# Optimization experiments

Measured on AMD Instinct MI355X. Metric: run time of the kernel, lower is better.

## Reference

```python
import jax, jax.numpy as jnp
import numpy as np

N = 20000      # total residues (nodes)
E = 320000     # contact edges
G = 16         # graphs in batch
D_IN = 1280    # ESM embedding dim
H = 256        # hidden channels (1=2=3)
C = 500        # GO classes
EPS = 1e-5


def setup_inputs() -> dict:
    key = jax.random.key(0)
    ks = jax.random.split(key, 16)
    s = 0.02
    return {
        "x": jax.random.normal(ks[0], (N, D_IN), jnp.float32),
        "edge_index": jax.random.randint(ks[1], (2, E), 0, N, jnp.int32),
        "edge_attr": jax.random.uniform(ks[2], (E, 1), jnp.float32),
        "batch": jnp.sort(jax.random.randint(ks[3], (N,), 0, G, jnp.int32)),
        "seq_emb": jax.random.normal(ks[4], (G, D_IN), jnp.float32),
        "W1": jax.random.normal(ks[5], (D_IN, H), jnp.float32) * s,
        "b1": jnp.zeros((H,), jnp.float32),
        "g1": jnp.ones((H,), jnp.float32),
        "be1": jnp.zeros((H,), jnp.float32),
        "W2": jax.random.normal(ks[6], (H, H), jnp.float32) * s,
        "b2": jnp.zeros((H,), jnp.float32),
        "g2": jnp.ones((H,), jnp.float32),
        "be2": jnp.zeros((H,), jnp.float32),
        "W3": jax.random.normal(ks[7], (H, H), jnp.float32) * s,
        "b3": jnp.zeros((H,), jnp.float32),
        "g3": jnp.ones((H,), jnp.float32),
        "be3": jnp.zeros((H,), jnp.float32),
        "fc1_w": jax.random.normal(ks[8], (D_IN, H), jnp.float32) * s,
        "fc1_b": jnp.zeros((H,), jnp.float32),
        "lin_w": jax.random.normal(ks[9], (H, C), jnp.float32) * s,
        "lin_b": jnp.zeros((C,), jnp.float32),
    }


def gcn_conv(x, row, col, ew, W, b):
    # PyG GCNConv: x' = D^{-1/2} (A + I) D^{-1/2} X W + b, with edge weights,
    # self-loops of weight 1, aggregation at target (col).
    xw = x @ W                                             # [N, H]
    deg = jax.ops.segment_sum(ew, col, num_segments=N) + 1.0
    dinv = jax.lax.rsqrt(deg)                              # [N]
    norm = dinv[row] * ew * dinv[col]                      # [E]
    agg = jax.ops.segment_sum(norm[:, None] * xw[row], col, num_segments=N)
    agg = agg + (dinv * dinv)[:, None] * xw                # self-loop term
    return agg + b


def batch_norm(x, g, b):
    # training-mode BN over the node dimension (biased variance, as torch)
    m = jnp.mean(x, axis=0)
    v = jnp.var(x, axis=0)
    return (x - m) * jax.lax.rsqrt(v + EPS) * g + b


def reference(x, edge_index, edge_attr, batch, seq_emb,
              W1, b1, g1, be1, W2, b2, g2, be2, W3, b3, g3, be3,
              fc1_w, fc1_b, lin_w, lin_b):
    row, col = edge_index[0], edge_index[1]
    ew = edge_attr[:, 0]

    h = batch_norm(jax.nn.relu(gcn_conv(x, row, col, ew, W1, b1)), g1, be1)
    h = batch_norm(jax.nn.relu(gcn_conv(h, row, col, ew, W2, b2)), g2, be2)
    h = batch_norm(gcn_conv(h, row, col, ew, W3, b3), g3, be3)

    # global_mean_pool over graphs
    sums = jax.ops.segment_sum(h, batch, num_segments=G)        # [G, H]
    cnt = jax.ops.segment_sum(jnp.ones((h.shape[0],), h.dtype), batch, num_segments=G)
    pooled = sums / jnp.maximum(cnt, 1.0)[:, None]

    y = seq_emb @ fc1_w + fc1_b                                 # [G, H]
    out = pooled + y
    # dropout skipped (eval mode)
    out = out @ lin_w + lin_b                                   # [G, C]
    return jax.nn.sigmoid(out)
```

## Files before the change

### kernel.cpp

```cpp
#include <hip/hip_runtime.h>
#include <hip/hip_bf16.h>
#include <math.h>

#define Nn 20000
#define En 320000
#define Gn 16
#define DINn 1280
#define Hn 256
#define Cn 500
#define EPSn 1e-5f
#define BNB 1024
#define SCB 256
#define SNB ((Nn + SCB - 1) / SCB)

typedef __attribute__((ext_vector_type(8))) short bf16x8;
typedef __attribute__((ext_vector_type(4))) float f32x4;

__device__ __forceinline__ float b2f(ushort u) {
    return __uint_as_float(((unsigned int)u) << 16);
}
__device__ __forceinline__ ushort f2b(float f) {
    __hip_bfloat16 h = __float2bfloat16(f);
    return *reinterpret_cast<ushort*>(&h);
}

#define GLOAD16(g, l) __builtin_amdgcn_global_load_lds( \
    (const __attribute__((address_space(1))) unsigned int*)(g), \
    (__attribute__((address_space(3))) unsigned int*)(l), 16, 0, 0)


__global__ void k_deg(const int* col, const float* ew, float* deg) {
    int e = blockIdx.x * blockDim.x + threadIdx.x;
    if (e < En) atomicAdd(&deg[col[e]], ew[e]);
}

__global__ void k_dinv(const float* deg, float* dinv, float* dinv2) {
    int i = blockIdx.x * blockDim.x + threadIdx.x;
    if (i < Nn) {
        float d = deg[i] + 1.0f;
        float r = rsqrtf(d);
        dinv[i] = r;
        dinv2[i] = 1.0f / d;
    }
}

__global__ void k_norm_count(const int* row, const int* col, const float* ew,
                             const float* dinv, float* normE, int* counts) {
    int e = blockIdx.x * blockDim.x + threadIdx.x;
    if (e < En) {
        int r = row[e], c = col[e];
        normE[e] = dinv[r] * ew[e] * dinv[c];
        atomicAdd(&counts[c], 1);
    }
}


__global__ __launch_bounds__(SCB) void k_scanA(const int* __restrict__ counts,
                                               int* __restrict__ excl,
                                               int* __restrict__ blocksum) {
    __shared__ int sd[SCB];
    int t = threadIdx.x, b = blockIdx.x;
    int i = b * SCB + t;
    int v = (i < Nn) ? counts[i] : 0;
    sd[t] = v;
    __syncthreads();
    #pragma unroll
    for (int o = 1; o < SCB; o <<= 1) {
        int tv = (t >= o) ? sd[t - o] : 0;
        __syncthreads();
        sd[t] += tv;
        __syncthreads();
    }
    if (i < Nn) excl[i] = sd[t] - v;
    if (t == SCB - 1) blocksum[b] = sd[t];
}

__global__ __launch_bounds__(128) void k_scanB(const int* __restrict__ blocksum,
                                               int* __restrict__ blockoff,
                                               int* __restrict__ offsets) {
    __shared__ int sd[128];
    int t = threadIdx.x;
    int v = (t < SNB) ? blocksum[t] : 0;
    sd[t] = v;
    __syncthreads();
    #pragma unroll
    for (int o = 1; o < 128; o <<= 1) {
        int tv = (t >= o) ? sd[t - o] : 0;
        __syncthreads();
        sd[t] += tv;
        __syncthreads();
    }
    if (t < SNB) blockoff[t] = sd[t] - v;
    if (t == SNB - 1) offsets[Nn] = sd[t];
}

__global__ __launch_bounds__(SCB) void k_scanC(const int* __restrict__ excl,
                                               const int* __restrict__ blockoff,
                                               int* __restrict__ offsets,
                                               int* __restrict__ cursor) {
    int b = blockIdx.x;
    int i = b * SCB + threadIdx.x;
    if (i < Nn) {
        int o = excl[i] + blockoff[b];
        offsets[i] = o;
        cursor[i] = o;
    }
}

__global__ void k_fill(const int* row, const int* col, const float* normE,
                       int* cursor, int* csr_row, float* csr_w) {
    int e = blockIdx.x * blockDim.x + threadIdx.x;
    if (e < En) {
        int c = col[e];
        int p = atomicAdd(&cursor[c], 1);
        csr_row[p] = row[e];
        csr_w[p] = normE[e];
    }
}


__global__ void k_gbounds(const int* __restrict__ batch, int* __restrict__ gstart) {
    int i = blockIdx.x * blockDim.x + threadIdx.x;
    if (i >= Nn) return;
    int b = batch[i];
    if (i == 0) {
        for (int g = 0; g <= b; g++) gstart[g] = 0;
    } else {
        int pb = batch[i - 1];
        for (int g = pb + 1; g <= b; g++) gstart[g] = i;
    }
    if (i == Nn - 1) {
        for (int g = b + 1; g <= Gn; g++) gstart[g] = Nn;
    }
}


__global__ __launch_bounds__(256) void k_x2bf(const float* __restrict__ x,
                                              ushort* __restrict__ xb) {
    size_t i = ((size_t)blockIdx.x * blockDim.x + threadIdx.x) * 8;
    const float4* xp = reinterpret_cast<const float4*>(&x[i]);
    float4 a = xp[0], b = xp[1];
    ushort t[8];
    t[0] = f2b(a.x); t[1] = f2b(a.y); t[2] = f2b(a.z); t[3] = f2b(a.w);
    t[4] = f2b(b.x); t[5] = f2b(b.y); t[6] = f2b(b.z); t[7] = f2b(b.w);
    *reinterpret_cast<uint4*>(&xb[i]) = *reinterpret_cast<uint4*>(&t[0]);
}


__global__ __launch_bounds__(256) void k_wt(const float* __restrict__ W,
                                            ushort* __restrict__ WT, int K) {
    __shared__ float tile[32][33];
    int k0 = blockIdx.x * 32, n0 = blockIdx.y * 32;
    int tx = threadIdx.x, ty = threadIdx.y;
    #pragma unroll
    for (int i = 0; i < 32; i += 8)
        tile[ty + i][tx] = W[(size_t)(k0 + ty + i) * Hn + n0 + tx];
    __syncthreads();
    #pragma unroll
    for (int i = 0; i < 32; i += 8)
        WT[(size_t)(n0 + ty + i) * K + k0 + tx] = f2b(tile[tx][ty + i]);
}


__global__ __launch_bounds__(256) void k_wtb(const float* __restrict__ W,
                                             const float* __restrict__ scaleA,
                                             const float* __restrict__ shiftA,
                                             ushort* __restrict__ WT,
                                             float* __restrict__ bv) {
    __shared__ float tile[32][33];
    int k0 = blockIdx.x * 32, n0 = blockIdx.y * 32;
    int tx = threadIdx.x, ty = threadIdx.y;
    #pragma unroll
    for (int i = 0; i < 32; i += 8)
        tile[ty + i][tx] = W[(size_t)(k0 + ty + i) * Hn + n0 + tx];
    __syncthreads();
    float sc = scaleA[k0 + tx], sh = shiftA[k0 + tx];
    #pragma unroll
    for (int i = 0; i < 32; i += 8) {
        float w = tile[tx][ty + i];
        WT[(size_t)(n0 + ty + i) * Hn + k0 + tx] = f2b(w * sc);
        float pb = w * sh;
        #pragma unroll
        for (int o = 16; o > 0; o >>= 1) pb += __shfl_down(pb, o, 32);
        if (tx == 0) atomicAdd(&bv[n0 + ty + i], pb);
    }
}


#define GBM 64
#define GBN 128
#define GBK 64

__global__ __launch_bounds__(256) void k_gemm_bf(
    const ushort* __restrict__ A, const ushort* __restrict__ BT,
    ushort* __restrict__ C, int M, int K)
{
    __shared__ ushort Asl[GBM][GBK];
    __shared__ ushort Bsl[GBN][GBK];
    const int bm = blockIdx.x * GBM;
    const int bn = blockIdx.y * GBN;
    const int tid = threadIdx.x;
    const int lane = tid & 63;
    const int wid = tid >> 6;
    const int wm = wid >> 1, wn = wid & 1;
    const int l15 = lane & 15, l16 = lane >> 4;

    const int lrow = lane >> 3;
    const int lcolb = 16 * ((lane & 7) ^ lrow);

    f32x4 acc[2][4] = {};
    const int nt = K / GBK;

    for (int t = 0; t < nt; t++) {
        const int k0 = t * GBK;
        #pragma unroll
        for (int c = 0; c < 2; c++) {
            int chunk = wid * 2 + c;
            int grow = bm + chunk * 8 + lrow;
            if (grow >= M) grow = M - 1;
            const char* src = (const char*)&A[(size_t)grow * K + k0] + lcolb;
            GLOAD16(src, &Asl[chunk * 8][0]);
        }
        #pragma unroll
        for (int c = 0; c < 4; c++) {
            int chunk = wid * 4 + c;
            int grow = bn + chunk * 8 + lrow;
            const char* src = (const char*)&BT[(size_t)grow * K + k0] + lcolb;
            GLOAD16(src, &Bsl[chunk * 8][0]);
        }
        __syncthreads();

        #pragma unroll
        for (int ks = 0; ks < 2; ks++) {
            bf16x8 afr[2], bfr[4];
            #pragma unroll
            for (int i = 0; i < 2; i++) {
                int r = wm * 32 + i * 16 + l15;
                int cb = (ks * 64 + l16 * 16) ^ ((r & 7) << 4);
                afr[i] = *reinterpret_cast<const bf16x8*>((const char*)&Asl[r][0] + cb);
            }
            #pragma unroll
            for (int j = 0; j < 4; j++) {
                int r = wn * 64 + j * 16 + l15;
                int cb = (ks * 64 + l16 * 16) ^ ((r & 7) << 4);
                bfr[j] = *reinterpret_cast<const bf16x8*>((const char*)&Bsl[r][0] + cb);
            }
            #pragma unroll
            for (int i = 0; i < 2; i++)
                #pragma unroll
                for (int j = 0; j < 4; j++)
                    acc[i][j] = __builtin_amdgcn_mfma_f32_16x16x32_bf16(afr[i], bfr[j], acc[i][j], 0, 0, 0);
        }
        __syncthreads();
    }

    #pragma unroll
    for (int i = 0; i < 2; i++) {
        #pragma unroll
        for (int r = 0; r < 4; r++) {
            int grow = bm + wm * 32 + i * 16 + l16 * 4 + r;
            if (grow < M) {
                #pragma unroll
                for (int j = 0; j < 4; j++)
                    C[(size_t)grow * Hn + bn + wn * 64 + j * 16 + l15] = f2b(acc[i][j][r]);
            }
        }
    }
}


__device__ __forceinline__ void agg_accum(float* acc, float w, const uint4& v) {
    unsigned int u;
    u = v.x; acc[0] += w * b2f((ushort)u); acc[1] += w * b2f((ushort)(u >> 16));
    u = v.y; acc[2] += w * b2f((ushort)u); acc[3] += w * b2f((ushort)(u >> 16));
    u = v.z; acc[4] += w * b2f((ushort)u); acc[5] += w * b2f((ushort)(u >> 16));
    u = v.w; acc[6] += w * b2f((ushort)u); acc[7] += w * b2f((ushort)(u >> 16));
}

__global__ __launch_bounds__(256) void k_agg(const ushort* __restrict__ xw,
                                             const int* __restrict__ offsets,
                                             const int* __restrict__ csr_row,
                                             const float* __restrict__ csr_w,
                                             const float* __restrict__ dinv2,
                                             const float* __restrict__ bias,
                                             const float* __restrict__ bv,
                                             ushort* __restrict__ outp, int do_relu) {
    int node = blockIdx.x * 8 + (threadIdx.x >> 5);
    int l32 = threadIdx.x & 31;
    int s = offsets[node], e = offsets[node + 1];
    const uint4* xw4 = reinterpret_cast<const uint4*>(xw);

    float acc[8] = {};
    float wsum = 0.f;
    int k = s;
    for (; k + 4 <= e; k += 4) {
        int r0 = csr_row[k],     r1 = csr_row[k + 1];
        int r2 = csr_row[k + 2], r3 = csr_row[k + 3];
        float w0 = csr_w[k],     w1 = csr_w[k + 1];
        float w2 = csr_w[k + 2], w3 = csr_w[k + 3];
        uint4 v0 = xw4[(size_t)r0 * 32 + l32];
        uint4 v1 = xw4[(size_t)r1 * 32 + l32];
        uint4 v2 = xw4[(size_t)r2 * 32 + l32];
        uint4 v3 = xw4[(size_t)r3 * 32 + l32];
        wsum += (w0 + w1) + (w2 + w3);
        agg_accum(acc, w0, v0);
        agg_accum(acc, w1, v1);
        agg_accum(acc, w2, v2);
        agg_accum(acc, w3, v3);
    }
    for (; k < e; k++) {
        int r = csr_row[k];
        float w = csr_w[k];
        uint4 v = xw4[(size_t)r * 32 + l32];
        wsum += w;
        agg_accum(acc, w, v);
    }
    float d2 = dinv2[node];
    wsum += d2;
    uint4 vs = xw4[(size_t)node * 32 + l32];
    agg_accum(acc, d2, vs);

    const float4* bp = reinterpret_cast<const float4*>(&bias[l32 * 8]);
    float4 bb0 = bp[0], bb1 = bp[1];
    acc[0] += bb0.x; acc[1] += bb0.y; acc[2] += bb0.z; acc[3] += bb0.w;
    acc[4] += bb1.x; acc[5] += bb1.y; acc[6] += bb1.z; acc[7] += bb1.w;
    if (bv) {
        const float4* vp = reinterpret_cast<const float4*>(&bv[l32 * 8]);
        float4 bv0 = vp[0], bv1 = vp[1];
        acc[0] += wsum * bv0.x; acc[1] += wsum * bv0.y;
        acc[2] += wsum * bv0.z; acc[3] += wsum * bv0.w;
        acc[4] += wsum * bv1.x; acc[5] += wsum * bv1.y;
        acc[6] += wsum * bv1.z; acc[7] += wsum * bv1.w;
    }
    if (do_relu) {
        #pragma unroll
        for (int q = 0; q < 8; q++) acc[q] = fmaxf(acc[q], 0.f);
    }
    uint4 o;
    o.x = (unsigned int)f2b(acc[0]) | ((unsigned int)f2b(acc[1]) << 16);
    o.y = (unsigned int)f2b(acc[2]) | ((unsigned int)f2b(acc[3]) << 16);
    o.z = (unsigned int)f2b(acc[4]) | ((unsigned int)f2b(acc[5]) << 16);
    o.w = (unsigned int)f2b(acc[6]) | ((unsigned int)f2b(acc[7]) << 16);
    reinterpret_cast<uint4*>(outp)[(size_t)node * 32 + l32] = o;
}


__global__ __launch_bounds__(256) void k_bnpart(const ushort* __restrict__ h,
                                                float* __restrict__ partial) {
    int f = threadIdx.x;
    int blk = blockIdx.x;
    float s = 0.0f, ss = 0.0f;
    for (int i = blk; i < Nn; i += BNB) {
        float v = b2f(h[(size_t)i * Hn + f]);
        s += v;
        ss += v * v;
    }
    partial[(size_t)blk * 512 + f] = s;
    partial[(size_t)blk * 512 + 256 + f] = ss;
}

__global__ __launch_bounds__(256) void k_bnred(const float* __restrict__ partial,
                                               float* __restrict__ p2) {
    int f = threadIdx.x;
    int b = blockIdx.x;
    int b0 = b * 64;
    float s = 0.0f, ss = 0.0f;
    for (int j = 0; j < 64; j++) {
        const float* p = &partial[(size_t)(b0 + j) * 512];
        s += p[f];
        ss += p[256 + f];
    }
    p2[b * 512 + f] = s;
    p2[b * 512 + 256 + f] = ss;
}

__global__ void k_bnfinal2(const float* __restrict__ p2, const float* g, const float* be,
                           float* scaleA, float* shiftA) {
    int f = threadIdx.x;
    float s = 0.f, ss = 0.f;
    #pragma unroll
    for (int j = 0; j < 16; j++) {
        s += p2[j * 512 + f];
        ss += p2[j * 512 + 256 + f];
    }
    float mean = s / (float)Nn;
    float var = ss / (float)Nn - mean * mean;
    float a = g[f] * rsqrtf(var + EPSn);
    scaleA[f] = a;
    shiftA[f] = be[f] - mean * a;
}


#define PCH 32

__global__ __launch_bounds__(256) void k_pool2(const ushort* __restrict__ h,
                                               const int* __restrict__ gstart,
                                               const float* __restrict__ scaleA,
                                               const float* __restrict__ shiftA,
                                               float* __restrict__ pooled) {
    int g = blockIdx.x;
    int chunk = blockIdx.y;
    int f = threadIdx.x;
    int s = gstart[g], e = gstart[g + 1];
    int len = e - s;
    if (len <= 0) return;
    int per = (len + PCH - 1) / PCH;
    int cs = s + chunk * per;
    int ce = cs + per; if (ce > e) ce = e;
    if (cs >= ce) return;
    float sc = scaleA[f], sh = shiftA[f];
    float acc = 0.0f;
    for (int i = cs; i < ce; i++)
        acc += b2f(h[(size_t)i * Hn + f]) * sc + sh;
    atomicAdd(&pooled[g * Hn + f], acc);
}


__global__ __launch_bounds__(256) void k_head1part(const float* __restrict__ seq_emb,
                                                   const float* __restrict__ fc1_w,
                                                   float* __restrict__ hpart) {
    int g = blockIdx.x;
    int kc = blockIdx.y;
    int j = threadIdx.x;
    const float* se = &seq_emb[(size_t)g * DINn + kc * 128];
    const float* w = &fc1_w[(size_t)kc * 128 * Hn + j];
    float acc = 0.0f;
    #pragma unroll 8
    for (int k = 0; k < 128; k++)
        acc += se[k] * w[(size_t)k * Hn];
    hpart[((size_t)g * 10 + kc) * Hn + j] = acc;
}

__global__ __launch_bounds__(256) void k_head2f(const float* __restrict__ hpart,
                                                const float* __restrict__ fc1_b,
                                                const float* __restrict__ pooled,
                                                const int* __restrict__ gstart,
                                                const float* __restrict__ lin_w,
                                                const float* __restrict__ lin_b,
                                                float* __restrict__ out) {
    __shared__ float pf[Hn];
    int g = blockIdx.x;
    int half = blockIdx.y;
    int j = threadIdx.x;
    float s = fc1_b[j];
    #pragma unroll
    for (int kc = 0; kc < 10; kc++)
        s += hpart[((size_t)g * 10 + kc) * Hn + j];
    float cntf = fmaxf((float)(gstart[g + 1] - gstart[g]), 1.0f);
    pf[j] = pooled[g * Hn + j] / cntf + s;
    __syncthreads();
    int c = half * 250 + j;
    if (j < 250) {
        float a2 = lin_b[c];
        #pragma unroll 8
        for (int k = 0; k < Hn; k++)
            a2 += pf[k] * lin_w[(size_t)k * Cn + c];
        out[g * Cn + c] = 1.0f / (1.0f + expf(-a2));
    }
}


extern "C" void kernel_launch(void* const* d_in, const int* in_sizes, int n_in,
                              void* d_out, int out_size, void* d_ws, size_t ws_size,
                              hipStream_t stream) {
    const float* x        = (const float*)d_in[0];
    const int*   eidx     = (const int*)d_in[1];
    const float* eattr    = (const float*)d_in[2];
    const int*   batch    = (const int*)d_in[3];
    const float* seq_emb  = (const float*)d_in[4];
    const float* W1 = (const float*)d_in[5];
    const float* b1 = (const float*)d_in[6];
    const float* g1 = (const float*)d_in[7];
    const float* be1 = (const float*)d_in[8];
    const float* W2 = (const float*)d_in[9];
    const float* b2 = (const float*)d_in[10];
    const float* g2 = (const float*)d_in[11];
    const float* be2 = (const float*)d_in[12];
    const float* W3 = (const float*)d_in[13];
    const float* b3 = (const float*)d_in[14];
    const float* g3 = (const float*)d_in[15];
    const float* be3 = (const float*)d_in[16];
    const float* fc1_w = (const float*)d_in[17];
    const float* fc1_b = (const float*)d_in[18];
    const float* lin_w = (const float*)d_in[19];
    const float* lin_b = (const float*)d_in[20];
    float* out = (float*)d_out;

    const int* row = eidx;
    const int* col = eidx + En;

    char* ws = (char*)d_ws;
    size_t off = 0;
    auto alloc = [&](size_t bytes) -> char* {
        char* p = ws + off;
        off += (bytes + 255) & ~(size_t)255;
        return p;
    };
    ushort* xb     = (ushort*)alloc((size_t)Nn * DINn * 2);
    ushort* xwb    = (ushort*)alloc((size_t)Nn * Hn * 2);
    ushort* hb     = (ushort*)alloc((size_t)Nn * Hn * 2);
    char*  zbase   = ws + off;
    float* deg     = (float*)alloc(Nn * 4);
    int*   counts  = (int*)alloc(Nn * 4);
    float* bvA     = (float*)alloc(Hn * 4);
    float* bvB     = (float*)alloc(Hn * 4);
    float* pooled  = (float*)alloc(Gn * Hn * 4);
    size_t zspan   = (size_t)((ws + off) - zbase);
    float* dinv    = (float*)alloc(Nn * 4);
    float* dinv2   = (float*)alloc(Nn * 4);
    float* normE   = (float*)alloc(En * 4);
    int*   offsets = (int*)alloc((Nn + 1) * 4);
    int*   cursor  = (int*)alloc(Nn * 4);
    int*   excl    = (int*)alloc(Nn * 4);
    int*   blocksum= (int*)alloc(SNB * 4);
    int*   blockoff= (int*)alloc(SNB * 4);
    int*   csr_row = (int*)alloc(En * 4);
    float* csr_w   = (float*)alloc(En * 4);
    float* scaleA  = (float*)alloc(Hn * 4);
    float* shiftA  = (float*)alloc(Hn * 4);
    int*   gstart  = (int*)alloc((Gn + 1) * 4);
    float* partial = (float*)alloc((size_t)BNB * 512 * 4);
    float* p2      = (float*)alloc(16 * 512 * 4);
    float* hpart   = (float*)alloc((size_t)Gn * 10 * Hn * 4);
    ushort* W1T    = (ushort*)alloc((size_t)Hn * DINn * 2);
    ushort* W2T    = (ushort*)alloc((size_t)Hn * Hn * 2);
    ushort* W3T    = (ushort*)alloc((size_t)Hn * Hn * 2);

    const int TB = 256;
    const int EB = (En + TB - 1) / TB;
    const int NB = (Nn + TB - 1) / TB;

    hipMemsetAsync(zbase, 0, zspan, stream);
    k_deg<<<EB, TB, 0, stream>>>(col, eattr, deg);
    k_dinv<<<NB, TB, 0, stream>>>(deg, dinv, dinv2);
    k_norm_count<<<EB, TB, 0, stream>>>(row, col, eattr, dinv, normE, counts);
    k_scanA<<<SNB, SCB, 0, stream>>>(counts, excl, blocksum);
    k_scanB<<<1, 128, 0, stream>>>(blocksum, blockoff, offsets);
    k_scanC<<<SNB, SCB, 0, stream>>>(excl, blockoff, offsets, cursor);
    k_fill<<<EB, TB, 0, stream>>>(row, col, normE, cursor, csr_row, csr_w);
    k_gbounds<<<NB, TB, 0, stream>>>(batch, gstart);
    k_x2bf<<<(Nn * DINn / 8) / 256, 256, 0, stream>>>(x, xb);
    k_wt<<<dim3(DINn / 32, Hn / 32), dim3(32, 8), 0, stream>>>(W1, W1T, DINn);

    dim3 gg((Nn + GBM - 1) / GBM, Hn / GBN);
    const int AGB = Nn / 8;

    k_gemm_bf<<<gg, 256, 0, stream>>>(xb, W1T, xwb, Nn, DINn);
    k_agg<<<AGB, 256, 0, stream>>>(xwb, offsets, csr_row, csr_w, dinv2, b1, nullptr, hb, 1);
    k_bnpart<<<BNB, Hn, 0, stream>>>(hb, partial);
    k_bnred<<<16, Hn, 0, stream>>>(partial, p2);
    k_bnfinal2<<<1, Hn, 0, stream>>>(p2, g1, be1, scaleA, shiftA);

    k_wtb<<<dim3(Hn / 32, Hn / 32), dim3(32, 8), 0, stream>>>(W2, scaleA, shiftA, W2T, bvA);
    k_gemm_bf<<<gg, 256, 0, stream>>>(hb, W2T, xwb, Nn, Hn);
    k_agg<<<AGB, 256, 0, stream>>>(xwb, offsets, csr_row, csr_w, dinv2, b2, bvA, hb, 1);
    k_bnpart<<<BNB, Hn, 0, stream>>>(hb, partial);
    k_bnred<<<16, Hn, 0, stream>>>(partial, p2);
    k_bnfinal2<<<1, Hn, 0, stream>>>(p2, g2, be2, scaleA, shiftA);

    k_wtb<<<dim3(Hn / 32, Hn / 32), dim3(32, 8), 0, stream>>>(W3, scaleA, shiftA, W3T, bvB);
    k_gemm_bf<<<gg, 256, 0, stream>>>(hb, W3T, xwb, Nn, Hn);
    k_agg<<<AGB, 256, 0, stream>>>(xwb, offsets, csr_row, csr_w, dinv2, b3, bvB, hb, 0);
    k_bnpart<<<BNB, Hn, 0, stream>>>(hb, partial);
    k_bnred<<<16, Hn, 0, stream>>>(partial, p2);
    k_bnfinal2<<<1, Hn, 0, stream>>>(p2, g3, be3, scaleA, shiftA);

    k_pool2<<<dim3(Gn, PCH), Hn, 0, stream>>>(hb, gstart, scaleA, shiftA, pooled);
    k_head1part<<<dim3(Gn, 10), Hn, 0, stream>>>(seq_emb, fc1_w, hpart);
    k_head2f<<<dim3(Gn, 2), Hn, 0, stream>>>(hpart, fc1_b, pooled, gstart, lin_w, lin_b, out);
}
```

Baseline: 296.5 us.

## Fuse batch-norm partial statistics into aggregation kernel and widen gather unroll

The aggregation kernel now computes per-block sum and sum-of-squares of its output features, reducing them across lanes and waves through shared memory, and writes one partial per block. This removes the separate k_bnpart pass, which re-read the whole hidden activation array three times. The neighbour gather loop is also unrolled to 8 edges, exposing more loads in flight. In exchange the partial buffer grows to 2500 blocks, the reduction uses 64 blocks, and the aggregation kernel takes on extra shared memory and a block-wide barrier. The statistics are now taken from fp32 values before the bf16 rounding that was previously applied.

```diff
diff --git a/kernel.cpp b/kernel.cpp
--- a/kernel.cpp
+++ b/kernel.cpp
@@ -9,9 +9,10 @@
 #define Hn 256
 #define Cn 500
 #define EPSn 1e-5f
-#define BNB 1024
 #define SCB 256
 #define SNB ((Nn + SCB - 1) / SCB)
+#define AGB (Nn / 8)
+#define RB 64
 
 typedef __attribute__((ext_vector_type(8))) short bf16x8;
 typedef __attribute__((ext_vector_type(4))) float f32x4;
@@ -284,7 +285,11 @@
                                              const float* __restrict__ dinv2,
                                              const float* __restrict__ bias,
                                              const float* __restrict__ bv,
-                                             ushort* __restrict__ outp, int do_relu) {
+                                             ushort* __restrict__ outp,
+                                             float* __restrict__ partial,
+                                             int do_relu) {
+    __shared__ float sls[4][Hn];
+    __shared__ float qls[4][Hn];
     int node = blockIdx.x * 8 + (threadIdx.x >> 5);
     int l32 = threadIdx.x & 31;
     int s = offsets[node], e = offsets[node + 1];
@@ -293,7 +298,30 @@
     float acc[8] = {};
     float wsum = 0.f;
     int k = s;
-    for (; k + 4 <= e; k += 4) {
+    for (; k + 8 <= e; k += 8) {
+        int r0 = csr_row[k],     r1 = csr_row[k + 1];
+        int r2 = csr_row[k + 2], r3 = csr_row[k + 3];
+        int r4 = csr_row[k + 4], r5 = csr_row[k + 5];
+        int r6 = csr_row[k + 6], r7 = csr_row[k + 7];
+        float w0 = csr_w[k],     w1 = csr_w[k + 1];
+        float w2 = csr_w[k + 2], w3 = csr_w[k + 3];
+        float w4 = csr_w[k + 4], w5 = csr_w[k + 5];
+        float w6 = csr_w[k + 6], w7 = csr_w[k + 7];
+        uint4 v0 = xw4[(size_t)r0 * 32 + l32];
+        uint4 v1 = xw4[(size_t)r1 * 32 + l32];
+        uint4 v2 = xw4[(size_t)r2 * 32 + l32];
+        uint4 v3 = xw4[(size_t)r3 * 32 + l32];
+        uint4 v4 = xw4[(size_t)r4 * 32 + l32];
+        uint4 v5 = xw4[(size_t)r5 * 32 + l32];
+        uint4 v6 = xw4[(size_t)r6 * 32 + l32];
+        uint4 v7 = xw4[(size_t)r7 * 32 + l32];
+        wsum += ((w0 + w1) + (w2 + w3)) + ((w4 + w5) + (w6 + w7));
+        agg_accum(acc, w0, v0); agg_accum(acc, w1, v1);
+        agg_accum(acc, w2, v2); agg_accum(acc, w3, v3);
+        agg_accum(acc, w4, v4); agg_accum(acc, w5, v5);
+        agg_accum(acc, w6, v6); agg_accum(acc, w7, v7);
+    }
+    if (k + 4 <= e) {
         int r0 = csr_row[k],     r1 = csr_row[k + 1];
         int r2 = csr_row[k + 2], r3 = csr_row[k + 3];
         float w0 = csr_w[k],     w1 = csr_w[k + 1];
@@ -303,10 +331,9 @@
         uint4 v2 = xw4[(size_t)r2 * 32 + l32];
         uint4 v3 = xw4[(size_t)r3 * 32 + l32];
         wsum += (w0 + w1) + (w2 + w3);
-        agg_accum(acc, w0, v0);
-        agg_accum(acc, w1, v1);
-        agg_accum(acc, w2, v2);
-        agg_accum(acc, w3, v3);
+        agg_accum(acc, w0, v0); agg_accum(acc, w1, v1);
+        agg_accum(acc, w2, v2); agg_accum(acc, w3, v3);
+        k += 4;
     }
     for (; k < e; k++) {
         int r = csr_row[k];
@@ -342,33 +369,40 @@
     o.z = (unsigned int)f2b(acc[4]) | ((unsigned int)f2b(acc[5]) << 16);
     o.w = (unsigned int)f2b(acc[6]) | ((unsigned int)f2b(acc[7]) << 16);
     reinterpret_cast<uint4*>(outp)[(size_t)node * 32 + l32] = o;
-}
-
-
-__global__ __launch_bounds__(256) void k_bnpart(const ushort* __restrict__ h,
-                                                float* __restrict__ partial) {
+
+    float s8[8], q8[8];
+    #pragma unroll
+    for (int q = 0; q < 8; q++) {
+        float a = acc[q];
+        float aa = a * a;
+        s8[q] = a + __shfl_xor(a, 32);
+        q8[q] = aa + __shfl_xor(aa, 32);
+    }
+    int wv = threadIdx.x >> 6;
+    if ((threadIdx.x & 63) < 32) {
+        #pragma unroll
+        for (int q = 0; q < 8; q++) {
+            sls[wv][l32 * 8 + q] = s8[q];
+            qls[wv][l32 * 8 + q] = q8[q];
+        }
+    }
+    __syncthreads();
     int f = threadIdx.x;
-    int blk = blockIdx.x;
-    float s = 0.0f, ss = 0.0f;
-    for (int i = blk; i < Nn; i += BNB) {
-        float v = b2f(h[(size_t)i * Hn + f]);
-        s += v;
-        ss += v * v;
-    }
-    partial[(size_t)blk * 512 + f] = s;
-    partial[(size_t)blk * 512 + 256 + f] = ss;
-}
+    float ps = (sls[0][f] + sls[1][f]) + (sls[2][f] + sls[3][f]);
+    float pq = (qls[0][f] + qls[1][f]) + (qls[2][f] + qls[3][f]);
+    partial[(size_t)blockIdx.x * 512 + f] = ps;
+    partial[(size_t)blockIdx.x * 512 + 256 + f] = pq;
+}
+
 
 __global__ __launch_bounds__(256) void k_bnred(const float* __restrict__ partial,
                                                float* __restrict__ p2) {
     int f = threadIdx.x;
     int b = blockIdx.x;
-    int b0 = b * 64;
     float s = 0.0f, ss = 0.0f;
-    for (int j = 0; j < 64; j++) {
-        const float* p = &partial[(size_t)(b0 + j) * 512];
-        s += p[f];
-        ss += p[256 + f];
+    for (int j = b; j < AGB; j += RB) {
+        s += partial[(size_t)j * 512 + f];
+        ss += partial[(size_t)j * 512 + 256 + f];
     }
     p2[b * 512 + f] = s;
     p2[b * 512 + 256 + f] = ss;
@@ -379,7 +413,7 @@
     int f = threadIdx.x;
     float s = 0.f, ss = 0.f;
     #pragma unroll
-    for (int j = 0; j < 16; j++) {
+    for (int j = 0; j < RB; j++) {
         s += p2[j * 512 + f];
         ss += p2[j * 512 + 256 + f];
     }
@@ -519,8 +553,8 @@
     float* scaleA  = (float*)alloc(Hn * 4);
     float* shiftA  = (float*)alloc(Hn * 4);
     int*   gstart  = (int*)alloc((Gn + 1) * 4);
-    float* partial = (float*)alloc((size_t)BNB * 512 * 4);
-    float* p2      = (float*)alloc(16 * 512 * 4);
+    float* partial = (float*)alloc((size_t)AGB * 512 * 4);
+    float* p2      = (float*)alloc(RB * 512 * 4);
     float* hpart   = (float*)alloc((size_t)Gn * 10 * Hn * 4);
     ushort* W1T    = (ushort*)alloc((size_t)Hn * DINn * 2);
     ushort* W2T    = (ushort*)alloc((size_t)Hn * Hn * 2);
@@ -543,26 +577,22 @@
     k_wt<<<dim3(DINn / 32, Hn / 32), dim3(32, 8), 0, stream>>>(W1, W1T, DINn);
 
     dim3 gg((Nn + GBM - 1) / GBM, Hn / GBN);
-    const int AGB = Nn / 8;
 
     k_gemm_bf<<<gg, 256, 0, stream>>>(xb, W1T, xwb, Nn, DINn);
-    k_agg<<<AGB, 256, 0, stream>>>(xwb, offsets, csr_row, csr_w, dinv2, b1, nullptr, hb, 1);
-    k_bnpart<<<BNB, Hn, 0, stream>>>(hb, partial);
-    k_bnred<<<16, Hn, 0, stream>>>(partial, p2);
+    k_agg<<<AGB, 256, 0, stream>>>(xwb, offsets, csr_row, csr_w, dinv2, b1, nullptr, hb, partial, 1);
+    k_bnred<<<RB, Hn, 0, stream>>>(partial, p2);
     k_bnfinal2<<<1, Hn, 0, stream>>>(p2, g1, be1, scaleA, shiftA);
 
     k_wtb<<<dim3(Hn / 32, Hn / 32), dim3(32, 8), 0, stream>>>(W2, scaleA, shiftA, W2T, bvA);
     k_gemm_bf<<<gg, 256, 0, stream>>>(hb, W2T, xwb, Nn, Hn);
-    k_agg<<<AGB, 256, 0, stream>>>(xwb, offsets, csr_row, csr_w, dinv2, b2, bvA, hb, 1);
-    k_bnpart<<<BNB, Hn, 0, stream>>>(hb, partial);
-    k_bnred<<<16, Hn, 0, stream>>>(partial, p2);
+    k_agg<<<AGB, 256, 0, stream>>>(xwb, offsets, csr_row, csr_w, dinv2, b2, bvA, hb, partial, 1);
+    k_bnred<<<RB, Hn, 0, stream>>>(partial, p2);
     k_bnfinal2<<<1, Hn, 0, stream>>>(p2, g2, be2, scaleA, shiftA);
 
     k_wtb<<<dim3(Hn / 32, Hn / 32), dim3(32, 8), 0, stream>>>(W3, scaleA, shiftA, W3T, bvB);
     k_gemm_bf<<<gg, 256, 0, stream>>>(hb, W3T, xwb, Nn, Hn);
-    k_agg<<<AGB, 256, 0, stream>>>(xwb, offsets, csr_row, csr_w, dinv2, b3, bvB, hb, 0);
-    k_bnpart<<<BNB, Hn, 0, stream>>>(hb, partial);
-    k_bnred<<<16, Hn, 0, stream>>>(partial, p2);
+    k_agg<<<AGB, 256, 0, stream>>>(xwb, offsets, csr_row, csr_w, dinv2, b3, bvB, hb, partial, 0);
+    k_bnred<<<RB, Hn, 0, stream>>>(partial, p2);
     k_bnfinal2<<<1, Hn, 0, stream>>>(p2, g3, be3, scaleA, shiftA);
 
     k_pool2<<<dim3(Gn, PCH), Hn, 0, stream>>>(hb, gstart, scaleA, shiftA, pooled);
```

New measurement: 316.9 us. 6.9% more time.
